# Kernel optimization log

Measured on AMD Instinct MI355X. Metric: run time of the kernel, lower is better.

Reference implementation:

```python
import jax, jax.numpy as jnp
import numpy as np

B, N, D, H = 8, 2048, 128, 4
DH = D // H
EPS_LN = 1e-5


def setup_inputs() -> dict:
    key = jax.random.key(0)
    ks = jax.random.split(key, 9)
    x = jax.random.normal(ks[0], (B, N, D), dtype=jnp.float32)
    u = jax.random.uniform(ks[1], (N, N), dtype=jnp.float32)
    adj = jnp.where(u > 0.5, u, 0.0)
    adj = adj.at[jnp.arange(N), jnp.arange(N)].set(1.0)
    W = jax.random.normal(ks[2], (D, D), dtype=jnp.float32) * (1.0 / np.sqrt(D))
    a_src = jax.random.normal(ks[3], (H, DH), dtype=jnp.float32) * 0.02
    a_dst = jax.random.normal(ks[4], (H, DH), dtype=jnp.float32) * 0.02
    Wo = jax.random.normal(ks[5], (D, D), dtype=jnp.float32) * (1.0 / np.sqrt(D))
    bo = jnp.zeros((D,), dtype=jnp.float32)
    gamma = jnp.ones((D,), dtype=jnp.float32)
    beta = jnp.zeros((D,), dtype=jnp.float32)
    return {"x": x, "adj_static": adj, "W": W, "a_src": a_src, "a_dst": a_dst,
            "Wo": Wo, "bo": bo, "gamma": gamma, "beta": beta}


def reference(x, adj_static, W, a_src, a_dst, Wo, bo, gamma, beta):
    # h: (B, H, N, DH)
    h = (x @ W.T).reshape(B, N, H, DH).transpose(0, 2, 1, 3)
    src = jnp.einsum('bhnd,hd->bhn', h, a_src)  # (B, H, N)
    dst = jnp.einsum('bhnd,hd->bhn', h, a_dst)  # (B, H, N)
    e = jax.nn.leaky_relu(src[..., :, None] + dst[..., None, :], 0.2)  # (B,H,N,N)
    logA = jnp.log(jnp.clip(adj_static, 1e-8))[None, None]
    mask = (adj_static > 0)[None, None]
    e = jnp.where(mask, e + logA, -jnp.inf)
    attn = jax.nn.softmax(e, axis=-1)  # dropout is identity in eval mode
    out = attn @ h  # (B, H, N, DH)
    out = out.transpose(0, 2, 1, 3).reshape(B, N, D)
    out = out @ Wo.T + bo
    y = x + out
    mu = jnp.mean(y, axis=-1, keepdims=True)
    var = jnp.mean(jnp.square(y - mu), axis=-1, keepdims=True)
    return (y - mu) * jax.lax.rsqrt(var + EPS_LN) * gamma + beta
```

## Files before the change

kernel.cpp:

```cpp
#include <hip/hip_runtime.h>

typedef short bf16x8 __attribute__((ext_vector_type(8)));
typedef _Float16 f16x8 __attribute__((ext_vector_type(8)));
typedef float f32x4  __attribute__((ext_vector_type(4)));
typedef float f32x2  __attribute__((ext_vector_type(2)));
typedef int   i32x4  __attribute__((ext_vector_type(4)));
typedef unsigned int u32x2 __attribute__((ext_vector_type(2)));

#define DEV static __device__ __forceinline__
#define LOG2E 1.4426950408889634f

DEV float bfu_to_f(unsigned short s) { return __builtin_bit_cast(float, (unsigned int)s << 16); }
DEV unsigned short f_to_bf(float f) {
  unsigned int u = __builtin_bit_cast(unsigned int, f);
  u += 0x7fffu + ((u >> 16) & 1u);
  return (unsigned short)(u >> 16);
}
DEV unsigned int pack_bf_rne(float lo, float hi) {
  return (unsigned int)f_to_bf(lo) | ((unsigned int)f_to_bf(hi) << 16);
}
DEV unsigned int pk_f16(float a, float b) {
  auto h = __builtin_amdgcn_cvt_pkrtz(a, b);
  return __builtin_bit_cast(unsigned int, h);
}
DEV unsigned short f_to_f16(float a) { return __builtin_bit_cast(unsigned short, (_Float16)a); }
DEV float nexp2(float x) {
#if __has_builtin(__builtin_amdgcn_exp2f)
  return __builtin_amdgcn_exp2f(x);
#else
  return exp2f(x);
#endif
}

DEV bool detect_f32(const void* adj) { return ((const float*)adj)[0] == 1.0f; }

template<bool F32> DEV float ldS(const void* p, size_t i) {
  if constexpr (F32) return ((const float*)p)[i];
  else               return bfu_to_f(((const unsigned short*)p)[i]);
}
template<bool F32> DEV void ld8f(const void* p, size_t i, float* o) {
  if constexpr (F32) {
    const float* f = (const float*)p + i;
    f32x4 a = *(const f32x4*)f, b = *(const f32x4*)(f + 4);
    o[0]=a[0]; o[1]=a[1]; o[2]=a[2]; o[3]=a[3];
    o[4]=b[0]; o[5]=b[1]; o[6]=b[2]; o[7]=b[3];
  } else {
    i32x4 w = *(const i32x4*)((const unsigned short*)p + i);
#pragma unroll
    for (int k = 0; k < 4; ++k) {
      unsigned int u = (unsigned int)w[k];
      o[2*k]   = __builtin_bit_cast(float, u << 16);
      o[2*k+1] = __builtin_bit_cast(float, u & 0xffff0000u);
    }
  }
}
template<bool F32> DEV bf16x8 ldfrag(const void* p, size_t i) {
  if constexpr (F32) {
    float o[8]; ld8f<true>(p, i, o);
    union { bf16x8 v; unsigned short u[8]; } r;
#pragma unroll
    for (int k = 0; k < 8; ++k) r.u[k] = f_to_bf(o[k]);
    return r.v;
  } else {
    return __builtin_bit_cast(bf16x8, *(const i32x4*)((const unsigned short*)p + i));
  }
}


__global__ __launch_bounds__(256) void k_prep(const void* __restrict__ adj,
                                              unsigned short* __restrict__ adjS) {
  const int tid = threadIdx.x, lane = tid & 63, w = tid >> 6;
  const int T = blockIdx.x * 4 + w;
  const int it = T >> 6, jt = T & 63;
  const int m = lane & 15, q = lane >> 4;
  const size_t src = (size_t)(it * 16 + m) * 2048 + jt * 32 + q * 8;
  float f[8];
  if (detect_f32(adj)) ld8f<true>(adj, src, f);
  else                 ld8f<false>(adj, src, f);
  i32x4 o;
#pragma unroll
  for (int k = 0; k < 4; ++k) o[k] = (int)pk_f16(f[2*k], f[2*k+1]);
  *(i32x4*)(adjS + (size_t)T * 512 + lane * 8) = o;
}

template<bool F32> DEV void k_h_body(const void* __restrict__ x, const void* __restrict__ W,
                                     unsigned short* __restrict__ vtS,
                                     unsigned short (&t_s)[16][136]) {
  const int tid = threadIdx.x, lane = tid & 63, wave = tid >> 6;
  const int nt = blockIdx.x >> 3, ct = blockIdx.x & 7;
  const int m = lane & 15, q = lane >> 4;
  bf16x8 wf[4];
#pragma unroll
  for (int k = 0; k < 4; ++k)
    wf[k] = ldfrag<F32>(W, (size_t)(ct * 16 + m) * 128 + q * 8 + k * 32);
#pragma unroll
  for (int s = 0; s < 2; ++s) {
    const int nsub = wave * 2 + s;
    const size_t xr = (size_t)(nt * 128 + nsub * 16 + m) * 128 + q * 8;
    f32x4 acc = {0.f, 0.f, 0.f, 0.f};
#pragma unroll
    for (int k = 0; k < 4; ++k)
      acc = __builtin_amdgcn_mfma_f32_16x16x32_bf16(ldfrag<F32>(x, xr + k * 32), wf[k],
                                                    acc, 0, 0, 0);
    u32x2 w2; w2[0] = pack_bf_rne(acc[0], acc[1]); w2[1] = pack_bf_rne(acc[2], acc[3]);
    *(u32x2*)&t_s[m][nsub * 16 + q * 4] = w2;
  }
  __syncthreads();
  const int row = tid >> 4, c8 = tid & 15;
  const int chg = ct * 16 + row, hh = chg >> 5, dloc = chg & 31;
  const int ng = nt * 128 + c8 * 8, b = ng >> 11, nl = ng & 2047;
  i32x4 v = *(const i32x4*)&t_s[row][c8 * 8];
  float f[8];
#pragma unroll
  for (int k = 0; k < 4; ++k) {
    unsigned int u = (unsigned int)v[k];
    f[2*k]   = __builtin_bit_cast(float, u << 16);
    f[2*k+1] = __builtin_bit_cast(float, u & 0xffff0000u);
  }
  i32x4 o;
#pragma unroll
  for (int k = 0; k < 4; ++k) o[k] = (int)pk_f16(f[2*k], f[2*k+1]);
  const int bh_ = b * 4 + hh;
  const size_t idx = ((size_t)(bh_ * 2 + (dloc >> 4)) * 64 + (nl >> 5)) * 512
                   + (((nl >> 3) & 3) * 16 + (dloc & 15)) * 8;
  *(i32x4*)(vtS + idx) = o;
}
__global__ __launch_bounds__(256) void k_h(const void* x, const void* W,
                                           unsigned short* vtS, const void* adj) {
  __shared__ __align__(16) unsigned short t_s[16][136];
  if (detect_f32(adj)) k_h_body<true>(x, W, vtS, t_s); else k_h_body<false>(x, W, vtS, t_s);
}

template<bool F32> DEV void k_sd_body(const unsigned short* __restrict__ vtS,
                                      const void* __restrict__ a_src, const void* __restrict__ a_dst,
                                      unsigned int* __restrict__ rvh,
                                      unsigned short* __restrict__ Fh,
                                      unsigned short* __restrict__ Hh) {
  const int t = blockIdx.x * 256 + threadIdx.x;
  const int n = t & 2047, bh = t >> 11, hh = bh & 3;
  const unsigned short* colp = vtS + ((size_t)(bh * 2) * 64 + (n >> 5)) * 512
                             + ((n >> 3) & 3) * 128 + (n & 7);
  float s = 0.f, d = 0.f;
#pragma unroll
  for (int dd = 0; dd < 32; ++dd) {
    const float v = (float)__builtin_bit_cast(_Float16,
                      colp[(dd >> 4) * 32768 + (dd & 15) * 8]);
    s += v * ldS<F32>(a_src, hh * 32 + dd);
    d += v * ldS<F32>(a_dst, hh * 32 + dd);
  }
  const float R = nexp2(-0.8f * LOG2E * s);
  const float F = nexp2(LOG2E * d);
  const float H = nexp2(0.2f * LOG2E * d);
  rvh[t] = pk_f16(R, R);
  Fh[t] = f_to_f16(F);
  Hh[t] = f_to_f16(H);
}
__global__ __launch_bounds__(256) void k_sd(const unsigned short* vtS, const void* a_src,
                                            const void* a_dst, unsigned int* rvh,
                                            unsigned short* Fh, unsigned short* Hh,
                                            const void* adj) {
  if (detect_f32(adj)) k_sd_body<true>(vtS, a_src, a_dst, rvh, Fh, Hh);
  else                 k_sd_body<false>(vtS, a_src, a_dst, rvh, Fh, Hh);
}

__global__ __launch_bounds__(256, 4) void k_attn(const unsigned short* __restrict__ adjS,
                                                 const unsigned short* __restrict__ vtS,
                                                 const unsigned int* __restrict__ rvh,
                                                 const unsigned short* __restrict__ Fh,
                                                 const unsigned short* __restrict__ Hh,
                                                 unsigned short* __restrict__ ao) {
  __shared__ __align__(16) float red[6144];
  const int tid = threadIdx.x, lane = tid & 63, wave = tid >> 6;
  const int swz = (blockIdx.x & 7) * 128 + (blockIdx.x >> 3);
  const int bh = swz & 31, iblk = swz >> 5;
  const int b = bh >> 2, hh = bh & 3;
  const int m = lane & 15, q = lane >> 4;
  const int i0 = iblk * 64;
  const int jq0 = wave * 16;

  const unsigned short* ap  = adjS + ((size_t)(iblk * 4) * 64 + jq0) * 512 + lane * 8;
  const unsigned short* vp0 = vtS + ((size_t)(bh * 2    ) * 64 + jq0) * 512 + lane * 8;
  const unsigned short* vp1 = vtS + ((size_t)(bh * 2 + 1) * 64 + jq0) * 512 + lane * 8;
  const unsigned short* fpF = Fh + (size_t)bh * 2048 + jq0 * 32 + q * 8;
  const unsigned short* fpH = Hh + (size_t)bh * 2048 + jq0 * 32 + q * 8;

  f16x8 R8[4];
#pragma unroll
  for (int it = 0; it < 4; ++it) {
    const unsigned int r = rvh[bh * 2048 + i0 + it * 16 + m];
    const i32x4 rb = {(int)r, (int)r, (int)r, (int)r};
    R8[it] = __builtin_bit_cast(f16x8, rb);
  }
  const i32x4 onev = {0x3C003C00, 0x3C003C00, 0x3C003C00, 0x3C003C00};
  const f16x8 ONE8 = __builtin_bit_cast(f16x8, onev);

  f32x4 accA[4], accB[4], accD[4];
#pragma unroll
  for (int it = 0; it < 4; ++it) {
    accA[it] = f32x4{0.f,0.f,0.f,0.f};
    accB[it] = f32x4{0.f,0.f,0.f,0.f};
    accD[it] = f32x4{0.f,0.f,0.f,0.f};
  }

#pragma unroll 4
  for (int j = 0; j < 16; ++j) {
    const i32x4 v0 = *(const i32x4*)(vp0 + j * 512);
    const i32x4 v1 = *(const i32x4*)(vp1 + j * 512);
    const i32x4 ff = *(const i32x4*)(fpF + j * 32);
    const i32x4 fh = *(const i32x4*)(fpH + j * 32);
    const f16x8 F8 = __builtin_bit_cast(f16x8, ff);
    const f16x8 H8 = __builtin_bit_cast(f16x8, fh);
    const f16x8 A0 = __builtin_bit_cast(f16x8, v0);
    const f16x8 A1 = __builtin_bit_cast(f16x8, v1);
#pragma unroll
    for (int it = 0; it < 4; ++it) {
      const i32x4 av = *(const i32x4*)(ap + it * 32768 + j * 512);
      const f16x8 w8 = __builtin_elementwise_max(F8, R8[it] * H8);
      const f16x8 p8 = __builtin_bit_cast(f16x8, av) * w8;
      accA[it] = __builtin_amdgcn_mfma_f32_16x16x32_f16(A0,   p8, accA[it], 0, 0, 0);
      accB[it] = __builtin_amdgcn_mfma_f32_16x16x32_f16(A1,   p8, accB[it], 0, 0, 0);
      accD[it] = __builtin_amdgcn_mfma_f32_16x16x32_f16(ONE8, p8, accD[it], 0, 0, 0);
    }
  }

  if (wave == 1 || wave == 3) {
    const int reg = (wave >> 1) * 3072;
#pragma unroll
    for (int it = 0; it < 4; ++it) {
      const int base = reg + (it * 64 + lane) * 12;
      *(f32x4*)&red[base]     = accA[it];
      *(f32x4*)&red[base + 4] = accB[it];
      red[base + 8] = accD[it][0];
    }
  }
  __syncthreads();
  if (wave == 0 || wave == 2) {
    const int reg = (wave >> 1) * 3072;
#pragma unroll
    for (int it = 0; it < 4; ++it) {
      const int base = reg + (it * 64 + lane) * 12;
      accA[it] += *(const f32x4*)&red[base];
      accB[it] += *(const f32x4*)&red[base + 4];
      accD[it][0] += red[base + 8];
    }
  }
  __syncthreads();
  if (wave == 2) {
#pragma unroll
    for (int it = 0; it < 4; ++it) {
      const int base = (it * 64 + lane) * 12;
      *(f32x4*)&red[base]     = accA[it];
      *(f32x4*)&red[base + 4] = accB[it];
      red[base + 8] = accD[it][0];
    }
  }
  __syncthreads();
  if (wave == 0) {
#pragma unroll
    for (int it = 0; it < 4; ++it) {
      const int base = (it * 64 + lane) * 12;
      const f32x4 a0 = accA[it] + *(const f32x4*)&red[base];
      const f32x4 a1 = accB[it] + *(const f32x4*)&red[base + 4];
      const float den = accD[it][0] + red[base + 8];
      const float inv = 1.f / fmaxf(den, 1e-20f);
      const int il = it * 16 + m;
      unsigned short* op = ao + ((size_t)(b * 2048) + i0 + il) * 128 + hh * 32 + q * 4;
      u32x2 w0, w1;
      w0[0] = pack_bf_rne(a0[0] * inv, a0[1] * inv);
      w0[1] = pack_bf_rne(a0[2] * inv, a0[3] * inv);
      w1[0] = pack_bf_rne(a1[0] * inv, a1[1] * inv);
      w1[1] = pack_bf_rne(a1[2] * inv, a1[3] * inv);
      *(u32x2*)op        = w0;
      *(u32x2*)(op + 16) = w1;
    }
  }
}

template<bool F32> DEV void k_out_body(const unsigned short* __restrict__ ao,
                                       const void* __restrict__ Wo, const void* __restrict__ bo,
                                       const void* __restrict__ x, const void* __restrict__ gamma,
                                       const void* __restrict__ beta, void* __restrict__ out,
                                       float (&y_s)[16][132]) {
  const int tid = threadIdx.x, lane = tid & 63, wave = tid >> 6;
  const int m = lane & 15, q = lane >> 4;
  const int rbase = blockIdx.x * 16;
  bf16x8 af[4];
#pragma unroll
  for (int k = 0; k < 4; ++k)
    af[k] = ldfrag<false>(ao, ((size_t)(rbase + m)) * 128 + q * 8 + k * 32);
  f32x4 acc[2] = {{0.f,0.f,0.f,0.f},{0.f,0.f,0.f,0.f}};
#pragma unroll
  for (int ct = 0; ct < 2; ++ct) {
    const size_t wrow = (size_t)(wave * 32 + ct * 16 + m) * 128 + q * 8;
#pragma unroll
    for (int k = 0; k < 4; ++k)
      acc[ct] = __builtin_amdgcn_mfma_f32_16x16x32_bf16(af[k], ldfrag<F32>(Wo, wrow + k * 32),
                                                        acc[ct], 0, 0, 0);
  }
#pragma unroll
  for (int ct = 0; ct < 2; ++ct) {
    const int c = wave * 32 + ct * 16 + m;
    const float bov = ldS<F32>(bo, c);
#pragma unroll
    for (int r = 0; r < 4; ++r) {
      const int row = q * 4 + r;
      y_s[row][c] = acc[ct][r] + bov + ldS<F32>(x, (size_t)(rbase + row) * 128 + c);
    }
  }
  __syncthreads();
  const int r = tid >> 4, c16 = tid & 15;
  float vals[8], sum = 0.f, sq = 0.f;
#pragma unroll
  for (int k = 0; k < 8; ++k) {
    const float v = y_s[r][c16 * 8 + k];
    vals[k] = v; sum += v; sq += v * v;
  }
#pragma unroll
  for (int msk = 1; msk < 16; msk <<= 1) {
    sum += __shfl_xor(sum, msk, 16);
    sq  += __shfl_xor(sq,  msk, 16);
  }
  const float mu  = sum * (1.f / 128.f);
  const float var = fmaxf(sq * (1.f / 128.f) - mu * mu, 0.f);
  const float rstd = rsqrtf(var + 1e-5f);
  float o[8];
#pragma unroll
  for (int k = 0; k < 8; ++k) {
    const int c = c16 * 8 + k;
    o[k] = (vals[k] - mu) * rstd * ldS<F32>(gamma, c) + ldS<F32>(beta, c);
  }
  const size_t obase = (size_t)(rbase + r) * 128 + c16 * 8;
  if constexpr (F32) {
    float* op = (float*)out + obase;
    f32x4 w0 = {o[0],o[1],o[2],o[3]}, w1 = {o[4],o[5],o[6],o[7]};
    *(f32x4*)op = w0; *(f32x4*)(op + 4) = w1;
  } else {
    union { unsigned short u[8]; i32x4 v; } ob;
#pragma unroll
    for (int k = 0; k < 8; ++k) ob.u[k] = f_to_bf(o[k]);
    *(i32x4*)((unsigned short*)out + obase) = ob.v;
  }
}
__global__ __launch_bounds__(256) void k_out(const unsigned short* ao, const void* Wo,
                                             const void* bo, const void* x, const void* gamma,
                                             const void* beta, void* out, const void* adj) {
  __shared__ __align__(16) float y_s[16][132];
  if (detect_f32(adj)) k_out_body<true>(ao, Wo, bo, x, gamma, beta, out, y_s);
  else                 k_out_body<false>(ao, Wo, bo, x, gamma, beta, out, y_s);
}

extern "C" void kernel_launch(void* const* d_in, const int* in_sizes, int n_in,
                              void* d_out, int out_size, void* d_ws, size_t ws_size,
                              hipStream_t stream) {
  const void* x     = d_in[0];
  const void* adj   = d_in[1];
  const void* W     = d_in[2];
  const void* a_src = d_in[3];
  const void* a_dst = d_in[4];
  const void* Wo    = d_in[5];
  const void* bo    = d_in[6];
  const void* gamma = d_in[7];
  const void* beta  = d_in[8];

  char* ws = (char*)d_ws;
  unsigned short* adjS  = (unsigned short*)ws;
  unsigned short* vtS   = (unsigned short*)(ws + 8388608);
  unsigned short* ao_ws = (unsigned short*)(ws + 12582912);
  unsigned int*   rvh   = (unsigned int*)(ws + 16777216);
  unsigned short* Fh    = (unsigned short*)(ws + 17039360);
  unsigned short* Hh    = (unsigned short*)(ws + 17170432);

  k_prep<<<2048, 256, 0, stream>>>(adj, adjS);
  k_h   <<<1024, 256, 0, stream>>>(x, W, vtS, adj);
  k_sd  <<<256,  256, 0, stream>>>(vtS, a_src, a_dst, rvh, Fh, Hh, adj);
  k_attn<<<1024, 256, 0, stream>>>(adjS, vtS, rvh, Fh, Hh, ao_ws);
  k_out <<<1024, 256, 0, stream>>>(ao_ws, Wo, bo, x, gamma, beta, d_out, adj);
}
```

Measured before the change: 175.9 us.

## Switch attention operands and adjacency to FP8 with fp8 MFMA

Adjacency, the transposed projected features and the attention probabilities are now stored and multiplied as FP8 (e4m3) using 16x16x32 fp8 MFMA, replacing f16. This halves the bytes streamed for adjS and vtS and the workspace footprint. The softmax weight is now computed in f32 pairs and then repacked to FP8, which adds conversion ALU work. The source/destination exponentials are packed as bf16 pairs, and the block swizzle in the attention kernel is removed. FP8 precision could hurt accuracy.

New measurement: 149.6 us. 1.18x faster.

```diff
diff --git a/kernel.cpp b/kernel.cpp
--- a/kernel.cpp
+++ b/kernel.cpp
@@ -1,7 +1,6 @@
 #include <hip/hip_runtime.h>
 
 typedef short bf16x8 __attribute__((ext_vector_type(8)));
-typedef _Float16 f16x8 __attribute__((ext_vector_type(8)));
 typedef float f32x4  __attribute__((ext_vector_type(4)));
 typedef float f32x2  __attribute__((ext_vector_type(2)));
 typedef int   i32x4  __attribute__((ext_vector_type(4)));
@@ -19,17 +18,21 @@
 DEV unsigned int pack_bf_rne(float lo, float hi) {
   return (unsigned int)f_to_bf(lo) | ((unsigned int)f_to_bf(hi) << 16);
 }
-DEV unsigned int pk_f16(float a, float b) {
-  auto h = __builtin_amdgcn_cvt_pkrtz(a, b);
-  return __builtin_bit_cast(unsigned int, h);
-}
-DEV unsigned short f_to_f16(float a) { return __builtin_bit_cast(unsigned short, (_Float16)a); }
+DEV float fplo(int u) { return __builtin_bit_cast(float, (unsigned int)u << 16); }
+DEV float fphi(int u) { return __builtin_bit_cast(float, (unsigned int)u & 0xffff0000u); }
 DEV float nexp2(float x) {
 #if __has_builtin(__builtin_amdgcn_exp2f)
   return __builtin_amdgcn_exp2f(x);
 #else
   return exp2f(x);
 #endif
+}
+template<bool HI> DEV unsigned int pk_fp8(float a, float b, unsigned int old) {
+  return __builtin_amdgcn_cvt_pk_fp8_f32(a, b, old, HI);
+}
+template<int W> DEV f32x2 upk_fp8(unsigned int w) {
+  auto r = __builtin_amdgcn_cvt_pk_f32_fp8(w, W);
+  f32x2 o; o[0] = r[0]; o[1] = r[1]; return o;
 }
 
 DEV bool detect_f32(const void* adj) { return ((const float*)adj)[0] == 1.0f; }
@@ -68,7 +71,7 @@
 
 
 __global__ __launch_bounds__(256) void k_prep(const void* __restrict__ adj,
-                                              unsigned short* __restrict__ adjS) {
+                                              unsigned char* __restrict__ adjF) {
   const int tid = threadIdx.x, lane = tid & 63, w = tid >> 6;
   const int T = blockIdx.x * 4 + w;
   const int it = T >> 6, jt = T & 63;
@@ -77,14 +80,14 @@
   float f[8];
   if (detect_f32(adj)) ld8f<true>(adj, src, f);
   else                 ld8f<false>(adj, src, f);
-  i32x4 o;
-#pragma unroll
-  for (int k = 0; k < 4; ++k) o[k] = (int)pk_f16(f[2*k], f[2*k+1]);
-  *(i32x4*)(adjS + (size_t)T * 512 + lane * 8) = o;
+  u32x2 o;
+  o[0] = pk_fp8<true>(f[2], f[3], pk_fp8<false>(f[0], f[1], 0u));
+  o[1] = pk_fp8<true>(f[6], f[7], pk_fp8<false>(f[4], f[5], 0u));
+  *(u32x2*)(adjF + (size_t)T * 512 + lane * 8) = o;
 }
 
 template<bool F32> DEV void k_h_body(const void* __restrict__ x, const void* __restrict__ W,
-                                     unsigned short* __restrict__ vtS,
+                                     unsigned char* __restrict__ vtF,
                                      unsigned short (&t_s)[16][136]) {
   const int tid = threadIdx.x, lane = tid & 63, wave = tid >> 6;
   const int nt = blockIdx.x >> 3, ct = blockIdx.x & 7;
@@ -117,82 +120,72 @@
     f[2*k]   = __builtin_bit_cast(float, u << 16);
     f[2*k+1] = __builtin_bit_cast(float, u & 0xffff0000u);
   }
-  i32x4 o;
-#pragma unroll
-  for (int k = 0; k < 4; ++k) o[k] = (int)pk_f16(f[2*k], f[2*k+1]);
+  u32x2 o;
+  o[0] = pk_fp8<true>(f[2], f[3], pk_fp8<false>(f[0], f[1], 0u));
+  o[1] = pk_fp8<true>(f[6], f[7], pk_fp8<false>(f[4], f[5], 0u));
   const int bh_ = b * 4 + hh;
-  const size_t idx = ((size_t)(bh_ * 2 + (dloc >> 4)) * 64 + (nl >> 5)) * 512
-                   + (((nl >> 3) & 3) * 16 + (dloc & 15)) * 8;
-  *(i32x4*)(vtS + idx) = o;
+  const size_t byte = ((size_t)(bh_ * 2 + (dloc >> 4)) * 64 + (nl >> 5)) * 512
+                    + (((nl >> 3) & 3) * 16 + (dloc & 15)) * 8;
+  *(u32x2*)(vtF + byte) = o;
 }
 __global__ __launch_bounds__(256) void k_h(const void* x, const void* W,
-                                           unsigned short* vtS, const void* adj) {
+                                           unsigned char* vtF, const void* adj) {
   __shared__ __align__(16) unsigned short t_s[16][136];
-  if (detect_f32(adj)) k_h_body<true>(x, W, vtS, t_s); else k_h_body<false>(x, W, vtS, t_s);
-}
-
-template<bool F32> DEV void k_sd_body(const unsigned short* __restrict__ vtS,
+  if (detect_f32(adj)) k_h_body<true>(x, W, vtF, t_s); else k_h_body<false>(x, W, vtF, t_s);
+}
+
+template<bool F32> DEV void k_sd_body(const unsigned char* __restrict__ vtF,
                                       const void* __restrict__ a_src, const void* __restrict__ a_dst,
-                                      unsigned int* __restrict__ rvh,
-                                      unsigned short* __restrict__ Fh,
-                                      unsigned short* __restrict__ Hh) {
+                                      float* __restrict__ rv, unsigned int* __restrict__ fhv) {
   const int t = blockIdx.x * 256 + threadIdx.x;
   const int n = t & 2047, bh = t >> 11, hh = bh & 3;
-  const unsigned short* colp = vtS + ((size_t)(bh * 2) * 64 + (n >> 5)) * 512
-                             + ((n >> 3) & 3) * 128 + (n & 7);
+  const unsigned char* colp = vtF + ((size_t)(bh * 2) * 64 + (n >> 5)) * 512
+                            + ((n >> 3) & 3) * 128 + (n & 7);
   float s = 0.f, d = 0.f;
 #pragma unroll
   for (int dd = 0; dd < 32; ++dd) {
-    const float v = (float)__builtin_bit_cast(_Float16,
-                      colp[(dd >> 4) * 32768 + (dd & 15) * 8]);
+    const float v = __builtin_amdgcn_cvt_f32_fp8(
+                      (int)colp[(dd >> 4) * 32768 + (dd & 15) * 8], 0);
     s += v * ldS<F32>(a_src, hh * 32 + dd);
     d += v * ldS<F32>(a_dst, hh * 32 + dd);
   }
-  const float R = nexp2(-0.8f * LOG2E * s);
+  rv[t] = nexp2(-0.8f * LOG2E * s);
   const float F = nexp2(LOG2E * d);
   const float H = nexp2(0.2f * LOG2E * d);
-  rvh[t] = pk_f16(R, R);
-  Fh[t] = f_to_f16(F);
-  Hh[t] = f_to_f16(H);
-}
-__global__ __launch_bounds__(256) void k_sd(const unsigned short* vtS, const void* a_src,
-                                            const void* a_dst, unsigned int* rvh,
-                                            unsigned short* Fh, unsigned short* Hh,
+  fhv[t] = pack_bf_rne(F, H);
+}
+__global__ __launch_bounds__(256) void k_sd(const unsigned char* vtF, const void* a_src,
+                                            const void* a_dst, float* rv, unsigned int* fhv,
                                             const void* adj) {
-  if (detect_f32(adj)) k_sd_body<true>(vtS, a_src, a_dst, rvh, Fh, Hh);
-  else                 k_sd_body<false>(vtS, a_src, a_dst, rvh, Fh, Hh);
-}
-
-__global__ __launch_bounds__(256, 4) void k_attn(const unsigned short* __restrict__ adjS,
-                                                 const unsigned short* __restrict__ vtS,
-                                                 const unsigned int* __restrict__ rvh,
-                                                 const unsigned short* __restrict__ Fh,
-                                                 const unsigned short* __restrict__ Hh,
+  if (detect_f32(adj)) k_sd_body<true>(vtF, a_src, a_dst, rv, fhv);
+  else                 k_sd_body<false>(vtF, a_src, a_dst, rv, fhv);
+}
+
+__global__ __launch_bounds__(256, 4) void k_attn(const unsigned char* __restrict__ adjF,
+                                                 const unsigned char* __restrict__ vtF,
+                                                 const float* __restrict__ rv,
+                                                 const unsigned int* __restrict__ fhv,
                                                  unsigned short* __restrict__ ao) {
   __shared__ __align__(16) float red[6144];
   const int tid = threadIdx.x, lane = tid & 63, wave = tid >> 6;
-  const int swz = (blockIdx.x & 7) * 128 + (blockIdx.x >> 3);
-  const int bh = swz & 31, iblk = swz >> 5;
+  const int bh = blockIdx.x & 31, iblk = blockIdx.x >> 5;
   const int b = bh >> 2, hh = bh & 3;
   const int m = lane & 15, q = lane >> 4;
   const int i0 = iblk * 64;
   const int jq0 = wave * 16;
 
-  const unsigned short* ap  = adjS + ((size_t)(iblk * 4) * 64 + jq0) * 512 + lane * 8;
-  const unsigned short* vp0 = vtS + ((size_t)(bh * 2    ) * 64 + jq0) * 512 + lane * 8;
-  const unsigned short* vp1 = vtS + ((size_t)(bh * 2 + 1) * 64 + jq0) * 512 + lane * 8;
-  const unsigned short* fpF = Fh + (size_t)bh * 2048 + jq0 * 32 + q * 8;
-  const unsigned short* fpH = Hh + (size_t)bh * 2048 + jq0 * 32 + q * 8;
-
-  f16x8 R8[4];
+  const unsigned char* ap  = adjF + ((size_t)(iblk * 4) * 64 + jq0) * 512 + lane * 8;
+  const unsigned char* vp0 = vtF + ((size_t)(bh * 2    ) * 64 + jq0) * 512 + lane * 8;
+  const unsigned char* vp1 = vtF + ((size_t)(bh * 2 + 1) * 64 + jq0) * 512 + lane * 8;
+  const unsigned int*  fp  = fhv + (size_t)bh * 2048 + jq0 * 32 + q * 8;
+
+  f32x2 Ri2[4];
 #pragma unroll
   for (int it = 0; it < 4; ++it) {
-    const unsigned int r = rvh[bh * 2048 + i0 + it * 16 + m];
-    const i32x4 rb = {(int)r, (int)r, (int)r, (int)r};
-    R8[it] = __builtin_bit_cast(f16x8, rb);
-  }
-  const i32x4 onev = {0x3C003C00, 0x3C003C00, 0x3C003C00, 0x3C003C00};
-  const f16x8 ONE8 = __builtin_bit_cast(f16x8, onev);
+    const float r = rv[bh * 2048 + i0 + it * 16 + m];
+    Ri2[it][0] = r; Ri2[it][1] = r;
+  }
+  const long Aones = 0x3838383838383838L;
 
   f32x4 accA[4], accB[4], accD[4];
 #pragma unroll
@@ -202,24 +195,33 @@
     accD[it] = f32x4{0.f,0.f,0.f,0.f};
   }
 
-#pragma unroll 4
+#pragma unroll
   for (int j = 0; j < 16; ++j) {
-    const i32x4 v0 = *(const i32x4*)(vp0 + j * 512);
-    const i32x4 v1 = *(const i32x4*)(vp1 + j * 512);
-    const i32x4 ff = *(const i32x4*)(fpF + j * 32);
-    const i32x4 fh = *(const i32x4*)(fpH + j * 32);
-    const f16x8 F8 = __builtin_bit_cast(f16x8, ff);
-    const f16x8 H8 = __builtin_bit_cast(f16x8, fh);
-    const f16x8 A0 = __builtin_bit_cast(f16x8, v0);
-    const f16x8 A1 = __builtin_bit_cast(f16x8, v1);
-#pragma unroll
-    for (int it = 0; it < 4; ++it) {
-      const i32x4 av = *(const i32x4*)(ap + it * 32768 + j * 512);
-      const f16x8 w8 = __builtin_elementwise_max(F8, R8[it] * H8);
-      const f16x8 p8 = __builtin_bit_cast(f16x8, av) * w8;
-      accA[it] = __builtin_amdgcn_mfma_f32_16x16x32_f16(A0,   p8, accA[it], 0, 0, 0);
-      accB[it] = __builtin_amdgcn_mfma_f32_16x16x32_f16(A1,   p8, accB[it], 0, 0, 0);
-      accD[it] = __builtin_amdgcn_mfma_f32_16x16x32_f16(ONE8, p8, accD[it], 0, 0, 0);
+    const long a0 = *(const long*)(vp0 + j * 512);
+    const long a1 = *(const long*)(vp1 + j * 512);
+    const i32x4 u0 = *(const i32x4*)(fp + j * 32);
+    const i32x4 u1 = *(const i32x4*)(fp + j * 32 + 4);
+    const f32x2 F0 = {fplo(u0[0]), fplo(u0[1])}, H0 = {fphi(u0[0]), fphi(u0[1])};
+    const f32x2 F1 = {fplo(u0[2]), fplo(u0[3])}, H1 = {fphi(u0[2]), fphi(u0[3])};
+    const f32x2 F2 = {fplo(u1[0]), fplo(u1[1])}, H2 = {fphi(u1[0]), fphi(u1[1])};
+    const f32x2 F3 = {fplo(u1[2]), fplo(u1[3])}, H3 = {fphi(u1[2]), fphi(u1[3])};
+#pragma unroll
+    for (int it = 0; it < 4; ++it) {
+      const u32x2 aw = *(const u32x2*)(ap + it * 32768 + j * 512);
+      f32x2 av0 = upk_fp8<0>(aw[0]), av1 = upk_fp8<1>(aw[0]);
+      f32x2 av2 = upk_fp8<0>(aw[1]), av3 = upk_fp8<1>(aw[1]);
+      f32x2 w0 = __builtin_elementwise_max(F0, Ri2[it] * H0);
+      f32x2 w1 = __builtin_elementwise_max(F1, Ri2[it] * H1);
+      f32x2 w2 = __builtin_elementwise_max(F2, Ri2[it] * H2);
+      f32x2 w3 = __builtin_elementwise_max(F3, Ri2[it] * H3);
+      f32x2 pv0 = av0 * w0, pv1 = av1 * w1, pv2 = av2 * w2, pv3 = av3 * w3;
+      u32x2 bp;
+      bp[0] = pk_fp8<true>(pv1[0], pv1[1], pk_fp8<false>(pv0[0], pv0[1], 0u));
+      bp[1] = pk_fp8<true>(pv3[0], pv3[1], pk_fp8<false>(pv2[0], pv2[1], 0u));
+      const long B = __builtin_bit_cast(long, bp);
+      accA[it] = __builtin_amdgcn_mfma_f32_16x16x32_fp8_fp8(a0,    B, accA[it], 0, 0, 0);
+      accB[it] = __builtin_amdgcn_mfma_f32_16x16x32_fp8_fp8(a1,    B, accB[it], 0, 0, 0);
+      accD[it] = __builtin_amdgcn_mfma_f32_16x16x32_fp8_fp8(Aones, B, accD[it], 0, 0, 0);
     }
   }
 
@@ -363,16 +365,15 @@
   const void* beta  = d_in[8];
 
   char* ws = (char*)d_ws;
-  unsigned short* adjS  = (unsigned short*)ws;
-  unsigned short* vtS   = (unsigned short*)(ws + 8388608);
-  unsigned short* ao_ws = (unsigned short*)(ws + 12582912);
-  unsigned int*   rvh   = (unsigned int*)(ws + 16777216);
-  unsigned short* Fh    = (unsigned short*)(ws + 17039360);
-  unsigned short* Hh    = (unsigned short*)(ws + 17170432);
-
-  k_prep<<<2048, 256, 0, stream>>>(adj, adjS);
-  k_h   <<<1024, 256, 0, stream>>>(x, W, vtS, adj);
-  k_sd  <<<256,  256, 0, stream>>>(vtS, a_src, a_dst, rvh, Fh, Hh, adj);
-  k_attn<<<1024, 256, 0, stream>>>(adjS, vtS, rvh, Fh, Hh, ao_ws);
+  unsigned char*  adjF  = (unsigned char*)ws;
+  unsigned char*  vtF   = (unsigned char*)(ws + 4194304);
+  unsigned short* ao_ws = (unsigned short*)(ws + 6291456);
+  float*          rv_ws = (float*)(ws + 10485760);
+  unsigned int*   fh_ws = (unsigned int*)(ws + 10747904);
+
+  k_prep<<<2048, 256, 0, stream>>>(adj, adjF);
+  k_h   <<<1024, 256, 0, stream>>>(x, W, vtF, adj);
+  k_sd  <<<256,  256, 0, stream>>>(vtF, a_src, a_dst, rv_ws, fh_ws, adj);
+  k_attn<<<1024, 256, 0, stream>>>(adjF, vtF, rv_ws, fh_ws, ao_ws);
   k_out <<<1024, 256, 0, stream>>>(ao_ws, Wo, bo, x, gamma, beta, d_out, adj);
 }
```
